# Kernel tuning notes

Measured on AMD Instinct MI355X. Metric: run time of the kernel, lower is better.

Reference implementation:

```python
import jax, jax.numpy as jnp
import numpy as np

KH, KW = 3, 3
STRIDE, PAD, DIL = 1, 1, 1


def setup_inputs() -> dict:
    key = jax.random.key(0)
    k1, k2, k3 = jax.random.split(key, 3)
    B, C, H, W, O = 8, 128, 64, 64, 128
    x = jax.random.normal(k1, (B, C, H, W), jnp.float32)
    # offset layout: [B, 2*K, Ho, Wo], pairs (dy, dx) per kernel tap
    offset = jax.random.normal(k2, (B, 2 * KH * KW, H, W), jnp.float32)
    n = C * KH * KW
    stdv = 1.0 / np.sqrt(n)
    weight = jax.random.uniform(k3, (O, C, KH, KW), jnp.float32, -stdv, stdv)
    bias = jnp.zeros((O,), jnp.float32)
    return {"x": x, "offset": offset, "weight": weight, "bias": bias}


def _deform_conv(x, offset, weight, bias):
    B, C, H, W = x.shape
    O = weight.shape[0]
    K = KH * KW
    Ho = (H + 2 * PAD - DIL * (KH - 1) - 1) // STRIDE + 1
    Wo = (W + 2 * PAD - DIL * (KW - 1) - 1) // STRIDE + 1

    off = offset.reshape(B, K, 2, Ho, Wo)  # (dy, dx) per tap

    # base sampling grid for each kernel tap: [K, Ho, Wo]
    hs = jnp.arange(Ho, dtype=jnp.float32) * STRIDE - PAD
    ws = jnp.arange(Wo, dtype=jnp.float32) * STRIDE - PAD
    ki = jnp.arange(KH, dtype=jnp.float32) * DIL
    kj = jnp.arange(KW, dtype=jnp.float32) * DIL
    base_y = (ki[:, None, None, None] + hs[None, None, :, None])  # [KH,1,Ho,1]
    base_x = (kj[None, :, None, None] + ws[None, None, None, :])  # [1,KW,1,Wo]
    base_y = jnp.broadcast_to(base_y, (KH, KW, Ho, Wo)).reshape(K, Ho, Wo)
    base_x = jnp.broadcast_to(base_x, (KH, KW, Ho, Wo)).reshape(K, Ho, Wo)

    py = base_y[None] + off[:, :, 0]  # [B,K,Ho,Wo]
    px = base_x[None] + off[:, :, 1]

    y0 = jnp.floor(py)
    x0 = jnp.floor(px)
    ly = py - y0  # fractional parts
    lx = px - x0
    y0i = y0.astype(jnp.int32)
    x0i = x0.astype(jnp.int32)

    flat = x.reshape(B, C, H * W)

    def gather(yi, xi, w):
        # zero outside the image (DCN zero-padding semantics)
        valid = (yi >= 0) & (yi < H) & (xi >= 0) & (xi < W)
        idx = jnp.clip(yi, 0, H - 1) * W + jnp.clip(xi, 0, W - 1)  # [B,K,Ho,Wo]
        g = jnp.take_along_axis(flat, idx.reshape(B, 1, -1), axis=2)
        g = g.reshape(B, C, K, Ho, Wo)
        wmask = (w * valid.astype(x.dtype))[:, None]  # [B,1,K,Ho,Wo]
        return g * wmask

    # bilinear accumulation over 4 corners -> im2col columns [B,C,K,Ho,Wo]
    cols = gather(y0i, x0i, (1 - ly) * (1 - lx))
    cols = cols + gather(y0i, x0i + 1, (1 - ly) * lx)
    cols = cols + gather(y0i + 1, x0i, ly * (1 - lx))
    cols = cols + gather(y0i + 1, x0i + 1, ly * lx)

    out = jnp.einsum('ock,bckhw->bohw', weight.reshape(O, C, K), cols)
    return out + bias[None, :, None, None]


def reference(x, offset, weight, bias):
    return _deform_conv(x, offset, weight, bias)
```

## Files before the change

kernel.cpp:

```cpp
#include <hip/hip_runtime.h>


#define BB 8
#define CC 128
#define HH 64
#define WW 64
#define OO 128
#define KTAPS 9

typedef __attribute__((ext_vector_type(8))) short bf16x8;
typedef __attribute__((ext_vector_type(4))) float f32x4;

__device__ __forceinline__ unsigned short f2bf(float f) {
    unsigned u = __float_as_uint(f);
    u += 0x7FFFu + ((u >> 16) & 1u);
    return (unsigned short)(u >> 16);
}
#if __has_builtin(__builtin_amdgcn_cvt_pk_bf16_f32)
typedef __attribute__((ext_vector_type(2))) __bf16 bf16x2_t;
__device__ __forceinline__ unsigned pack2bf(float lo, float hi) {
    bf16x2_t v = __builtin_amdgcn_cvt_pk_bf16_f32(lo, hi);
    unsigned r;
    __builtin_memcpy(&r, &v, 4);
    return r;
}
#else
__device__ __forceinline__ unsigned pack2bf(float lo, float hi) {
    return (unsigned)f2bf(lo) | ((unsigned)f2bf(hi) << 16);
}
#endif
__device__ __forceinline__ float bflo(unsigned p) { return __uint_as_float(p << 16); }
__device__ __forceinline__ float bfhi(unsigned p) { return __uint_as_float(p & 0xFFFF0000u); }

__device__ __forceinline__ void gload_lds16(const void* g, void* l) {
#if __has_builtin(__builtin_amdgcn_global_load_lds)
    auto* lp = reinterpret_cast<__attribute__((address_space(3))) unsigned*>(
        reinterpret_cast<uintptr_t>(l));
    auto* gp = reinterpret_cast<const __attribute__((address_space(1))) unsigned*>(
        reinterpret_cast<uintptr_t>(g));
    __builtin_amdgcn_global_load_lds(gp, lp, 16, 0, 0);
#else
    const int lane = threadIdx.x & 63;
    *reinterpret_cast<uint4*>(reinterpret_cast<char*>(l) + lane * 16) =
        *reinterpret_cast<const uint4*>(reinterpret_cast<const char*>(g) + lane * 16);
#endif
}

__global__ __launch_bounds__(256)
void prep_kernel(const float* __restrict__ x, const float* __restrict__ wgt,
                 unsigned short* __restrict__ xt, unsigned short* __restrict__ wpk) {
    const int t = threadIdx.x;
    if (blockIdx.x < 512) {
        __shared__ float tile[WW * 132];
        const int b = blockIdx.x >> 6;
        const int h = blockIdx.x & 63;
        const float* src = x + ((size_t)b * CC * HH + h) * WW;
        {
            const int wq = t & 15;
            const int cb = t >> 4;
#pragma unroll
            for (int it = 0; it < 8; ++it) {
                const int c = it * 16 + cb;
                const float4 v = *reinterpret_cast<const float4*>(src + (size_t)c * (HH * WW) + wq * 4);
                tile[(wq * 4 + 0) * 132 + c] = v.x;
                tile[(wq * 4 + 1) * 132 + c] = v.y;
                tile[(wq * 4 + 2) * 132 + c] = v.z;
                tile[(wq * 4 + 3) * 132 + c] = v.w;
            }
        }
        __syncthreads();
        unsigned short* dst = xt + ((size_t)b * HH + h) * WW * CC;
        {
            const int cg = t & 15;
            const int wb = t >> 4;
#pragma unroll
            for (int it = 0; it < 4; ++it) {
                const int w = it * 16 + wb;
                const float* tp = &tile[w * 132 + cg * 8];
                uint4 p;
                p.x = pack2bf(tp[0], tp[1]);
                p.y = pack2bf(tp[2], tp[3]);
                p.z = pack2bf(tp[4], tp[5]);
                p.w = pack2bf(tp[6], tp[7]);
                *reinterpret_cast<uint4*>(&dst[(size_t)w * CC + cg * 8]) = p;
            }
        }
    } else {
        const int id   = (blockIdx.x - 512) * 256 + t;
        const int lane = id & 63;
        const int frag = id >> 6;
        const int nt   = frag & 7;
        const int c0q  = (frag >> 3) & 3;
        const int tap  = frag >> 5;
        const int o    = (nt << 4) + (lane & 15);
        const int c    = (c0q << 5) + ((lane >> 4) << 3);
        const float* s = wgt + ((size_t)o * CC + c) * KTAPS + tap;
        unsigned u[4];
#pragma unroll
        for (int j = 0; j < 4; ++j)
            u[j] = pack2bf(s[(2 * j) * KTAPS], s[(2 * j + 1) * KTAPS]);
        *reinterpret_cast<uint4*>(wpk + (size_t)frag * 512 + lane * 8) =
            make_uint4(u[0], u[1], u[2], u[3]);
    }
}

__device__ __forceinline__ void decode_tap(const float2* __restrict__ sLL,
                                           const short2* __restrict__ sYX,
                                           int rec, int extra,
                                           unsigned& o00, unsigned& o01,
                                           unsigned& o10, unsigned& o11,
                                           float& w00, float& w01,
                                           float& w10, float& w11) {
    const float2 ll = sLL[rec];
    const short2 yx = sYX[rec];
    const int y0 = yx.x, x0 = yx.y;
    const int y1 = y0 + 1, x1 = x0 + 1;
    const float ly = ll.x, lx = ll.y;
    const bool vy0 = ((unsigned)y0 < (unsigned)HH);
    const bool vy1 = ((unsigned)y1 < (unsigned)HH);
    const bool vx0 = ((unsigned)x0 < (unsigned)WW);
    const bool vx1 = ((unsigned)x1 < (unsigned)WW);
    w00 = (vy0 && vx0) ? (1.f - ly) * (1.f - lx) : 0.f;
    w01 = (vy0 && vx1) ? (1.f - ly) * lx         : 0.f;
    w10 = (vy1 && vx0) ? ly * (1.f - lx)         : 0.f;
    w11 = (vy1 && vx1) ? ly * lx                 : 0.f;
    const int cy0 = min(max(y0, 0), HH - 1);
    const int cy1 = min(max(y1, 0), HH - 1);
    const int cx0 = min(max(x0, 0), WW - 1);
    const int cx1 = min(max(x1, 0), WW - 1);
    o00 = (unsigned)((((cy0 << 6) + cx0) << 8) + extra);
    o01 = (unsigned)((((cy0 << 6) + cx1) << 8) + extra);
    o10 = (unsigned)((((cy1 << 6) + cx0) << 8) + extra);
    o11 = (unsigned)((((cy1 << 6) + cx1) << 8) + extra);
}

__global__ __launch_bounds__(512, 4)
void dcn_mfma_kernel(const unsigned short* __restrict__ xt,
                     const unsigned short* __restrict__ wpk,
                     const float* __restrict__ offset,
                     const float* __restrict__ bias,
                     float* __restrict__ out) {
    __shared__ __align__(16) char smem[6912 + 2 * 32768];
    float2* sLL = reinterpret_cast<float2*>(smem);
    short2* sYX = reinterpret_cast<short2*>(smem + 4608);
    char*   Bb  = smem + 6912;

    const int t = threadIdx.x;
    const int bid0 = blockIdx.x;
    const int nid  = ((bid0 & 7) << 6) | (bid0 >> 3);
    const int b    = nid >> 6;
    const int ho   = nid & 63;

    const int lane = t & 63;
    const int wave = t >> 6;
    const int mt   = wave & 3;
    const int grp  = wave >> 2;
    const int lm   = lane & 15;
    const int quad = lane >> 4;
    const int lane16 = lane * 16;
    const int extra = (grp << 7) + (quad << 4);
    const char* xb = (const char*)(xt + (size_t)b * HH * WW * CC);
    const char* wb = (const char*)wpk;
    const int fb_grp = grp << 1;

    for (int s = t; s < KTAPS * 64; s += 512) {
        const int k  = s >> 6;
        const int wo = s & 63;
        const int ki = k / 3;
        const int kj = k - ki * 3;
        const float dy = offset[(((size_t)b * 18 + 2 * k    ) * 64 + ho) * 64 + wo];
        const float dx = offset[(((size_t)b * 18 + 2 * k + 1) * 64 + ho) * 64 + wo];
        const float py = (float)(ho - 1 + ki) + dy;
        const float px = (float)(wo - 1 + kj) + dx;
        const float y0f = floorf(py);
        const float x0f = floorf(px);
        sLL[s] = make_float2(py - y0f, px - x0f);
        sYX[s] = make_short2((short)(int)y0f, (short)(int)x0f);
    }

    {
        const char* src = wb + wave * 4096 + lane16;
        char* dst = Bb + wave * 4096;
#pragma unroll
        for (int j = 0; j < 4; ++j)
            gload_lds16(src + j * 1024, dst + j * 1024);
    }
    __syncthreads();

    f32x4 acc[8];
#pragma unroll
    for (int nt = 0; nt < 8; ++nt) acc[nt] = (f32x4){0.f, 0.f, 0.f, 0.f};

    unsigned o00, o01, o10, o11;
    float w00, w01, w10, w11;
    decode_tap(sLL, sYX, (mt << 4) + lm, extra, o00, o01, o10, o11, w00, w01, w10, w11);
    uint4 a00 = *reinterpret_cast<const uint4*>(xb + o00);
    uint4 a01 = *reinterpret_cast<const uint4*>(xb + o01);
    uint4 a10 = *reinterpret_cast<const uint4*>(xb + o10);
    uint4 a11 = *reinterpret_cast<const uint4*>(xb + o11);

    int cur = 0;
    for (int tap = 0; tap < KTAPS; ++tap) {
        if (tap < KTAPS - 1) {
            const char* src = wb + (tap + 1) * 32768 + wave * 4096 + lane16;
            char* dst = Bb + ((cur ^ 1) << 15) + wave * 4096;
#pragma unroll
            for (int j = 0; j < 4; ++j)
                gload_lds16(src + j * 1024, dst + j * 1024);
        }

        const char* bslice = Bb + (cur << 15);
#pragma unroll
        for (int cq = 0; cq < 2; ++cq) {
            uint4 bfr[8];
            const char* brow = bslice + (((fb_grp + cq) << 13) + lane16);
#pragma unroll
            for (int nt = 0; nt < 8; ++nt)
                bfr[nt] = *reinterpret_cast<const uint4*>(brow + (nt << 10));

            uint4 n00, n01, n10, n11;
            unsigned no00 = 0, no01 = 0, no10 = 0, no11 = 0;
            float nw00 = 0.f, nw01 = 0.f, nw10 = 0.f, nw11 = 0.f;
            if (cq == 0) {
                n00 = *reinterpret_cast<const uint4*>(xb + o00 + 64);
                n01 = *reinterpret_cast<const uint4*>(xb + o01 + 64);
                n10 = *reinterpret_cast<const uint4*>(xb + o10 + 64);
                n11 = *reinterpret_cast<const uint4*>(xb + o11 + 64);
            } else if (tap < KTAPS - 1) {
                decode_tap(sLL, sYX, ((tap + 1) << 6) + (mt << 4) + lm, extra,
                           no00, no01, no10, no11, nw00, nw01, nw10, nw11);
                n00 = *reinterpret_cast<const uint4*>(xb + no00);
                n01 = *reinterpret_cast<const uint4*>(xb + no01);
                n10 = *reinterpret_cast<const uint4*>(xb + no10);
                n11 = *reinterpret_cast<const uint4*>(xb + no11);
            }

            const unsigned* u00 = reinterpret_cast<const unsigned*>(&a00);
            const unsigned* u01 = reinterpret_cast<const unsigned*>(&a01);
            const unsigned* u10 = reinterpret_cast<const unsigned*>(&a10);
            const unsigned* u11 = reinterpret_cast<const unsigned*>(&a11);
            unsigned afu[4];
#pragma unroll
            for (int j = 0; j < 4; ++j) {
                const float rl = w00 * bflo(u00[j]) + w01 * bflo(u01[j])
                               + w10 * bflo(u10[j]) + w11 * bflo(u11[j]);
                const float rh = w00 * bfhi(u00[j]) + w01 * bfhi(u01[j])
                               + w10 * bfhi(u10[j]) + w11 * bfhi(u11[j]);
                afu[j] = pack2bf(rl, rh);
            }
            bf16x8 afrag;
            __builtin_memcpy(&afrag, afu, 16);
#pragma unroll
            for (int nt = 0; nt < 8; ++nt) {
                bf16x8 bfrag;
                __builtin_memcpy(&bfrag, &bfr[nt], 16);
                acc[nt] = __builtin_amdgcn_mfma_f32_16x16x32_bf16(afrag, bfrag, acc[nt], 0, 0, 0);
            }

            if (cq == 0) {
                a00 = n00; a01 = n01; a10 = n10; a11 = n11;
            } else if (tap < KTAPS - 1) {
                a00 = n00; a01 = n01; a10 = n10; a11 = n11;
                o00 = no00; o01 = no01; o10 = no10; o11 = no11;
                w00 = nw00; w01 = nw01; w10 = nw10; w11 = nw11;
            }
        }

        __syncthreads();
        cur ^= 1;
    }

    float* scrA = reinterpret_cast<float*>(Bb);
    float* scrM = scrA + mt * (128 * 20);
    if (grp == 0) {
#pragma unroll
        for (int nt = 0; nt < 8; ++nt) {
            const int o_l = (nt << 4) + lm;
            *reinterpret_cast<float4*>(&scrM[o_l * 20 + (quad << 2)]) =
                make_float4(acc[nt][0], acc[nt][1], acc[nt][2], acc[nt][3]);
        }
    }
    __syncthreads();
    if (grp == 1) {
#pragma unroll
        for (int nt = 0; nt < 8; ++nt) {
            const int o_l = (nt << 4) + lm;
            float4* p = reinterpret_cast<float4*>(&scrM[o_l * 20 + (quad << 2)]);
            float4 f = *p;
            f.x += acc[nt][0]; f.y += acc[nt][1];
            f.z += acc[nt][2]; f.w += acc[nt][3];
            *p = f;
        }
    }
    __syncthreads();
    {
        const int o = (grp << 6) + lane;
        const float bv = bias[o];
        float* op = out + (((size_t)(b * OO + o) * HH + ho) << 6) + (mt << 4);
        const float* sr = scrM + o * 20;
#pragma unroll
        for (int j = 0; j < 4; ++j) {
            const float4 f = *reinterpret_cast<const float4*>(sr + j * 4);
            *reinterpret_cast<float4*>(op + j * 4) =
                make_float4(f.x + bv, f.y + bv, f.z + bv, f.w + bv);
        }
    }
}

extern "C" void kernel_launch(void* const* d_in, const int* in_sizes, int n_in,
                              void* d_out, int out_size, void* d_ws, size_t ws_size,
                              hipStream_t stream) {
    const float* x      = (const float*)d_in[0];
    const float* offset = (const float*)d_in[1];
    const float* wgt    = (const float*)d_in[2];
    const float* bias   = (const float*)d_in[3];
    float* out = (float*)d_out;

    unsigned short* xt  = (unsigned short*)d_ws;
    unsigned short* wpk = xt + (size_t)BB * HH * WW * CC;

    hipLaunchKernelGGL(prep_kernel, dim3(512 + 72), dim3(256), 0, stream, x, wgt, xt, wpk);
    hipLaunchKernelGGL(dcn_mfma_kernel, dim3(BB * HH), dim3(512), 0, stream,
                       xt, wpk, offset, bias, out);
}
```

Before: 121.9 us.

## Split output rows into half-width tiles with four-way channel split-K

Each block now covers half an output row (32 pixels) instead of a full row, so twice as many blocks launch. The eight waves are split into 2 pixel tiles by 4 channel groups, each wave handling one 32-channel chunk per tap. The weight tile per tap is staged in two 16 KB halves with a single-buffer ping-pong, and partial sums are reduced across channel groups through LDS in a tree. Smaller shared memory and launch bounds of 6 aim at higher occupancy and better load balance. The cost is more barriers per tap, extra reduction traffic, and redundant weight loads across blocks.

```diff
diff --git a/kernel.cpp b/kernel.cpp
--- a/kernel.cpp
+++ b/kernel.cpp
@@ -89,10 +89,11 @@
         const int id   = (blockIdx.x - 512) * 256 + t;
         const int lane = id & 63;
         const int frag = id >> 6;
-        const int nt   = frag & 7;
-        const int c0q  = (frag >> 3) & 3;
+        const int ntl  = frag & 3;
+        const int c0q  = (frag >> 2) & 3;
+        const int nh   = (frag >> 4) & 1;
         const int tap  = frag >> 5;
-        const int o    = (nt << 4) + (lane & 15);
+        const int o    = ((nh << 2) + ntl) * 16 + (lane & 15);
         const int c    = (c0q << 5) + ((lane >> 4) << 3);
         const float* s = wgt + ((size_t)o * CC + c) * KTAPS + tap;
         unsigned u[4];
@@ -134,38 +135,59 @@
     o11 = (unsigned)((((cy1 << 6) + cx1) << 8) + extra);
 }
 
-__global__ __launch_bounds__(512, 4)
+__device__ __forceinline__ bf16x8 blend4(const uint4& a00, const uint4& a01,
+                                         const uint4& a10, const uint4& a11,
+                                         float w00, float w01, float w10, float w11) {
+    const unsigned* u00 = reinterpret_cast<const unsigned*>(&a00);
+    const unsigned* u01 = reinterpret_cast<const unsigned*>(&a01);
+    const unsigned* u10 = reinterpret_cast<const unsigned*>(&a10);
+    const unsigned* u11 = reinterpret_cast<const unsigned*>(&a11);
+    unsigned afu[4];
+#pragma unroll
+    for (int j = 0; j < 4; ++j) {
+        const float rl = w00 * bflo(u00[j]) + w01 * bflo(u01[j])
+                       + w10 * bflo(u10[j]) + w11 * bflo(u11[j]);
+        const float rh = w00 * bfhi(u00[j]) + w01 * bfhi(u01[j])
+                       + w10 * bfhi(u10[j]) + w11 * bfhi(u11[j]);
+        afu[j] = pack2bf(rl, rh);
+    }
+    bf16x8 afrag;
+    __builtin_memcpy(&afrag, afu, 16);
+    return afrag;
+}
+
+__global__ __launch_bounds__(512, 6)
 void dcn_mfma_kernel(const unsigned short* __restrict__ xt,
                      const unsigned short* __restrict__ wpk,
                      const float* __restrict__ offset,
                      const float* __restrict__ bias,
                      float* __restrict__ out) {
-    __shared__ __align__(16) char smem[6912 + 2 * 32768];
+    __shared__ __align__(16) char smem[3584 + 2 * 16384];
     float2* sLL = reinterpret_cast<float2*>(smem);
-    short2* sYX = reinterpret_cast<short2*>(smem + 4608);
-    char*   Bb  = smem + 6912;
+    short2* sYX = reinterpret_cast<short2*>(smem + 2304);
+    char*   Bb  = smem + 3584;
 
     const int t = threadIdx.x;
     const int bid0 = blockIdx.x;
-    const int nid  = ((bid0 & 7) << 6) | (bid0 >> 3);
-    const int b    = nid >> 6;
-    const int ho   = nid & 63;
+    const int nid  = ((bid0 & 7) << 7) | (bid0 >> 3);
+    const int b    = nid >> 7;
+    const int ho   = (nid >> 1) & 63;
+    const int wo0  = (nid & 1) << 5;
 
     const int lane = t & 63;
     const int wave = t >> 6;
-    const int mt   = wave & 3;
-    const int grp  = wave >> 2;
+    const int mt   = wave & 1;
+    const int kgrp = wave >> 1;
     const int lm   = lane & 15;
     const int quad = lane >> 4;
     const int lane16 = lane * 16;
-    const int extra = (grp << 7) + (quad << 4);
+    const int extra = (kgrp << 6) + (quad << 4);
     const char* xb = (const char*)(xt + (size_t)b * HH * WW * CC);
     const char* wb = (const char*)wpk;
-    const int fb_grp = grp << 1;
-
-    for (int s = t; s < KTAPS * 64; s += 512) {
-        const int k  = s >> 6;
-        const int wo = s & 63;
+
+    if (t < KTAPS * 32) {
+        const int k  = t >> 5;
+        const int wo = wo0 + (t & 31);
         const int ki = k / 3;
         const int kj = k - ki * 3;
         const float dy = offset[(((size_t)b * 18 + 2 * k    ) * 64 + ho) * 64 + wo];
@@ -174,16 +196,15 @@
         const float px = (float)(wo - 1 + kj) + dx;
         const float y0f = floorf(py);
         const float x0f = floorf(px);
-        sLL[s] = make_float2(py - y0f, px - x0f);
-        sYX[s] = make_short2((short)(int)y0f, (short)(int)x0f);
+        sLL[t] = make_float2(py - y0f, px - x0f);
+        sYX[t] = make_short2((short)(int)y0f, (short)(int)x0f);
     }
 
     {
-        const char* src = wb + wave * 4096 + lane16;
-        char* dst = Bb + wave * 4096;
-#pragma unroll
-        for (int j = 0; j < 4; ++j)
-            gload_lds16(src + j * 1024, dst + j * 1024);
+        const char* src = wb + wave * 2048 + lane16;
+        char* dst = Bb + wave * 2048;
+        gload_lds16(src, dst);
+        gload_lds16(src + 1024, dst + 1024);
     }
     __syncthreads();
 
@@ -199,110 +220,89 @@
     uint4 a10 = *reinterpret_cast<const uint4*>(xb + o10);
     uint4 a11 = *reinterpret_cast<const uint4*>(xb + o11);
 
-    int cur = 0;
     for (int tap = 0; tap < KTAPS; ++tap) {
+        {
+            const char* src = wb + ((size_t)((tap << 1) + 1) << 14) + wave * 2048 + lane16;
+            char* dst = Bb + 16384 + wave * 2048;
+            gload_lds16(src, dst);
+            gload_lds16(src + 1024, dst + 1024);
+        }
+        const bf16x8 afrag = blend4(a00, a01, a10, a11, w00, w01, w10, w11);
         if (tap < KTAPS - 1) {
-            const char* src = wb + (tap + 1) * 32768 + wave * 4096 + lane16;
-            char* dst = Bb + ((cur ^ 1) << 15) + wave * 4096;
-#pragma unroll
-            for (int j = 0; j < 4; ++j)
-                gload_lds16(src + j * 1024, dst + j * 1024);
-        }
-
-        const char* bslice = Bb + (cur << 15);
-#pragma unroll
-        for (int cq = 0; cq < 2; ++cq) {
-            uint4 bfr[8];
-            const char* brow = bslice + (((fb_grp + cq) << 13) + lane16);
-#pragma unroll
-            for (int nt = 0; nt < 8; ++nt)
-                bfr[nt] = *reinterpret_cast<const uint4*>(brow + (nt << 10));
-
-            uint4 n00, n01, n10, n11;
-            unsigned no00 = 0, no01 = 0, no10 = 0, no11 = 0;
-            float nw00 = 0.f, nw01 = 0.f, nw10 = 0.f, nw11 = 0.f;
-            if (cq == 0) {
-                n00 = *reinterpret_cast<const uint4*>(xb + o00 + 64);
-                n01 = *reinterpret_cast<const uint4*>(xb + o01 + 64);
-                n10 = *reinterpret_cast<const uint4*>(xb + o10 + 64);
-                n11 = *reinterpret_cast<const uint4*>(xb + o11 + 64);
-            } else if (tap < KTAPS - 1) {
-                decode_tap(sLL, sYX, ((tap + 1) << 6) + (mt << 4) + lm, extra,
-                           no00, no01, no10, no11, nw00, nw01, nw10, nw11);
-                n00 = *reinterpret_cast<const uint4*>(xb + no00);
-                n01 = *reinterpret_cast<const uint4*>(xb + no01);
-                n10 = *reinterpret_cast<const uint4*>(xb + no10);
-                n11 = *reinterpret_cast<const uint4*>(xb + no11);
+            decode_tap(sLL, sYX, ((tap + 1) << 5) + (mt << 4) + lm, extra,
+                       o00, o01, o10, o11, w00, w01, w10, w11);
+            a00 = *reinterpret_cast<const uint4*>(xb + o00);
+            a01 = *reinterpret_cast<const uint4*>(xb + o01);
+            a10 = *reinterpret_cast<const uint4*>(xb + o10);
+            a11 = *reinterpret_cast<const uint4*>(xb + o11);
+        }
+        {
+            const char* brow = Bb + (kgrp << 12) + lane16;
+#pragma unroll
+            for (int ntl = 0; ntl < 4; ++ntl) {
+                bf16x8 bfrag;
+                const uint4 bv = *reinterpret_cast<const uint4*>(brow + (ntl << 10));
+                __builtin_memcpy(&bfrag, &bv, 16);
+                acc[ntl] = __builtin_amdgcn_mfma_f32_16x16x32_bf16(afrag, bfrag, acc[ntl], 0, 0, 0);
             }
-
-            const unsigned* u00 = reinterpret_cast<const unsigned*>(&a00);
-            const unsigned* u01 = reinterpret_cast<const unsigned*>(&a01);
-            const unsigned* u10 = reinterpret_cast<const unsigned*>(&a10);
-            const unsigned* u11 = reinterpret_cast<const unsigned*>(&a11);
-            unsigned afu[4];
-#pragma unroll
-            for (int j = 0; j < 4; ++j) {
-                const float rl = w00 * bflo(u00[j]) + w01 * bflo(u01[j])
-                               + w10 * bflo(u10[j]) + w11 * bflo(u11[j]);
-                const float rh = w00 * bfhi(u00[j]) + w01 * bfhi(u01[j])
-                               + w10 * bfhi(u10[j]) + w11 * bfhi(u11[j]);
-                afu[j] = pack2bf(rl, rh);
+        }
+        __syncthreads();
+
+        if (tap < KTAPS - 1) {
+            const char* src = wb + ((size_t)((tap + 1) << 1) << 14) + wave * 2048 + lane16;
+            char* dst = Bb + wave * 2048;
+            gload_lds16(src, dst);
+            gload_lds16(src + 1024, dst + 1024);
+        }
+        {
+            const char* brow = Bb + 16384 + (kgrp << 12) + lane16;
+#pragma unroll
+            for (int ntl = 0; ntl < 4; ++ntl) {
+                bf16x8 bfrag;
+                const uint4 bv = *reinterpret_cast<const uint4*>(brow + (ntl << 10));
+                __builtin_memcpy(&bfrag, &bv, 16);
+                acc[4 + ntl] = __builtin_amdgcn_mfma_f32_16x16x32_bf16(afrag, bfrag, acc[4 + ntl], 0, 0, 0);
             }
-            bf16x8 afrag;
-            __builtin_memcpy(&afrag, afu, 16);
-#pragma unroll
-            for (int nt = 0; nt < 8; ++nt) {
-                bf16x8 bfrag;
-                __builtin_memcpy(&bfrag, &bfr[nt], 16);
-                acc[nt] = __builtin_amdgcn_mfma_f32_16x16x32_bf16(afrag, bfrag, acc[nt], 0, 0, 0);
-            }
-
-            if (cq == 0) {
-                a00 = n00; a01 = n01; a10 = n10; a11 = n11;
-            } else if (tap < KTAPS - 1) {
-                a00 = n00; a01 = n01; a10 = n10; a11 = n11;
-                o00 = no00; o01 = no01; o10 = no10; o11 = no11;
-                w00 = nw00; w01 = nw01; w10 = nw10; w11 = nw11;
-            }
-        }
-
+        }
         __syncthreads();
-        cur ^= 1;
-    }
-
-    float* scrA = reinterpret_cast<float*>(Bb);
-    float* scrM = scrA + mt * (128 * 20);
-    if (grp == 0) {
+    }
+
+    char* scr = Bb;
+    if (kgrp & 1) {
+        char* w = scr + ((((kgrp >> 1) << 1) + mt) << 13) + lane16;
+#pragma unroll
+        for (int nt = 0; nt < 8; ++nt)
+            *reinterpret_cast<f32x4*>(w + (nt << 10)) = acc[nt];
+    }
+    __syncthreads();
+    if (!(kgrp & 1)) {
+        const char* r = scr + ((((kgrp >> 1) << 1) + mt) << 13) + lane16;
 #pragma unroll
         for (int nt = 0; nt < 8; ++nt) {
-            const int o_l = (nt << 4) + lm;
-            *reinterpret_cast<float4*>(&scrM[o_l * 20 + (quad << 2)]) =
-                make_float4(acc[nt][0], acc[nt][1], acc[nt][2], acc[nt][3]);
+            const f32x4 p = *reinterpret_cast<const f32x4*>(r + (nt << 10));
+            acc[nt] += p;
         }
     }
     __syncthreads();
-    if (grp == 1) {
+    if (kgrp == 2) {
+        char* w = scr + ((size_t)mt << 13) + lane16;
+#pragma unroll
+        for (int nt = 0; nt < 8; ++nt)
+            *reinterpret_cast<f32x4*>(w + (nt << 10)) = acc[nt];
+    }
+    __syncthreads();
+    if (kgrp == 0) {
+        const char* r = scr + ((size_t)mt << 13) + lane16;
 #pragma unroll
         for (int nt = 0; nt < 8; ++nt) {
-            const int o_l = (nt << 4) + lm;
-            float4* p = reinterpret_cast<float4*>(&scrM[o_l * 20 + (quad << 2)]);
-            float4 f = *p;
-            f.x += acc[nt][0]; f.y += acc[nt][1];
-            f.z += acc[nt][2]; f.w += acc[nt][3];
-            *p = f;
-        }
-    }
-    __syncthreads();
-    {
-        const int o = (grp << 6) + lane;
-        const float bv = bias[o];
-        float* op = out + (((size_t)(b * OO + o) * HH + ho) << 6) + (mt << 4);
-        const float* sr = scrM + o * 20;
-#pragma unroll
-        for (int j = 0; j < 4; ++j) {
-            const float4 f = *reinterpret_cast<const float4*>(sr + j * 4);
-            *reinterpret_cast<float4*>(op + j * 4) =
-                make_float4(f.x + bv, f.y + bv, f.z + bv, f.w + bv);
+            const f32x4 p = *reinterpret_cast<const f32x4*>(r + (nt << 10));
+            const f32x4 s = acc[nt] + p;
+            const int o = (nt << 4) + lm;
+            const float bv = bias[o];
+            float* op = out + (((size_t)(b * OO + o) * HH + ho) << 6)
+                      + wo0 + (mt << 4) + (quad << 2);
+            *reinterpret_cast<float4*>(op) =
+                make_float4(s[0] + bv, s[1] + bv, s[2] + bv, s[3] + bv);
         }
     }
 }
@@ -320,6 +320,6 @@
     unsigned short* wpk = xt + (size_t)BB * HH * WW * CC;
 
     hipLaunchKernelGGL(prep_kernel, dim3(512 + 72), dim3(256), 0, stream, x, wgt, xt, wpk);
-    hipLaunchKernelGGL(dcn_mfma_kernel, dim3(BB * HH), dim3(512), 0, stream,
+    hipLaunchKernelGGL(dcn_mfma_kernel, dim3(2 * BB * HH), dim3(512), 0, stream,
                        xt, wpk, offset, bias, out);
 }
```

After: 131.8 us. 8.1% more time.
